# Performance work log

Measured on AMD Instinct MI355X. Metric: run time of the kernel, lower is better.

The kernel has to match this reference:

```python
import jax, jax.numpy as jnp
import numpy as np

N_NODES = 100000
N_EDGES = 3200000
D_IN, D_HID, N_CLASSES = 128, 16, 10


def gcn_conv(x, src, dst, W, b, num_nodes):
    # PyG GCNConv: h = W x; add self-loops; symmetric deg^-1/2 normalization; scatter-sum; + bias
    h = x @ W                                        # [N, d_out]
    loops = jnp.arange(num_nodes, dtype=src.dtype)
    s = jnp.concatenate([src, loops])                # [E+N]
    d = jnp.concatenate([dst, loops])                # [E+N]
    deg = jax.ops.segment_sum(jnp.ones_like(d, dtype=h.dtype), d, num_segments=num_nodes)
    dinv = jax.lax.rsqrt(jnp.maximum(deg, 1.0))      # self-loops guarantee deg >= 1
    norm = dinv[s] * dinv[d]                         # [E+N]
    msg = h[s] * norm[:, None]                       # gather + scale
    out = jax.ops.segment_sum(msg, d, num_segments=num_nodes)
    return out + b


def setup_inputs() -> dict:
    key = jax.random.key(0)
    k1, k2, k3, k4, k5, k6 = jax.random.split(key, 6)
    x = jax.random.normal(k1, (N_NODES, D_IN), dtype=jnp.float32)
    edge_index = jax.random.randint(k2, (2, N_EDGES), 0, N_NODES, dtype=jnp.int32)
    W1 = jax.random.normal(k3, (D_IN, D_HID), dtype=jnp.float32) / np.sqrt(D_IN)
    b1 = jnp.zeros((D_HID,), dtype=jnp.float32)
    W2 = jax.random.normal(k4, (D_HID, N_CLASSES), dtype=jnp.float32) / np.sqrt(D_HID)
    b2 = jnp.zeros((N_CLASSES,), dtype=jnp.float32)
    return {"x": x, "edge_index": edge_index, "W1": W1, "b1": b1, "W2": W2, "b2": b2}


def reference(x, edge_index, W1, b1, W2, b2):
    num_nodes = x.shape[0]
    src, dst = edge_index[0], edge_index[1]
    h = jax.nn.relu(gcn_conv(x, src, dst, W1, b1, num_nodes))
    # dropout is identity in eval mode
    h = gcn_conv(h, src, dst, W2, b2, num_nodes)
    return jax.nn.log_softmax(h, axis=1)
```

## Files before the change

kernel.cpp:

```cpp
#include <hip/hip_runtime.h>
#include <hip/hip_fp16.h>
#include <math.h>

#define NNODES 100000
#define BSH 7
#define NBUCK 782
#define CAP 5120
#define EPB 8192
#define PBT 512
#define EPT 16

typedef __attribute__((ext_vector_type(8))) _Float16 f16x8;
typedef __attribute__((ext_vector_type(2))) __fp16 fp16x2;
typedef __attribute__((ext_vector_type(4))) float f32x4;

__device__ inline __half2 shfl_xor_h2(__half2 v, int m) {
    union { __half2 h; int i; } u;
    u.h = v;
    u.i = __shfl_xor(u.i, m);
    return u.h;
}

__global__ void k_zero(int* __restrict__ p, int n) {
    int t = threadIdx.x;
    if (t < n) p[t] = 0;
}

__global__ __launch_bounds__(512) void k_part(const int* __restrict__ src, const int* __restrict__ dst,
                                              int* __restrict__ bcur, unsigned int* __restrict__ part,
                                              int E) {
    __shared__ int h[NBUCK];
    __shared__ int gb[NBUCK];
    int t = threadIdx.x;
    for (int i = t; i < NBUCK; i += PBT) h[i] = 0;
    __syncthreads();
    int base = blockIdx.x * EPB;
    int n = min(EPB, E - base);
    const int2* src2 = (const int2*)(src + base);
    const int2* dst2 = (const int2*)(dst + base);
    unsigned ev[EPT];
    int bv[EPT];
#pragma unroll
    for (int p = 0; p < EPT / 2; ++p) {
        int i2 = t + p * PBT;
        if (2 * i2 < n) {
            int2 s2 = src2[i2];
            int2 d2 = dst2[i2];
            bv[2 * p]     = d2.x >> BSH;
            ev[2 * p]     = (unsigned)s2.x | ((unsigned)(d2.x & 127) << 17);
            bv[2 * p + 1] = d2.y >> BSH;
            ev[2 * p + 1] = (unsigned)s2.y | ((unsigned)(d2.y & 127) << 17);
            atomicAdd(&h[bv[2 * p]], 1);
            atomicAdd(&h[bv[2 * p + 1]], 1);
        } else {
            bv[2 * p] = -1;
            bv[2 * p + 1] = -1;
        }
    }
    __syncthreads();
    for (int bq = t; bq < NBUCK; bq += PBT) {
        int c = h[bq];
        if (c) gb[bq] = atomicAdd(&bcur[bq], c);
        h[bq] = 0;
    }
    __syncthreads();
#pragma unroll
    for (int p = 0; p < EPT; ++p) {
        if (bv[p] >= 0) {
            int pos = atomicAdd(&h[bv[p]], 1);
            int g = gb[bv[p]] + pos;
            if (g < CAP) part[(size_t)bv[p] * CAP + g] = ev[p];
        }
    }
}

__global__ __launch_bounds__(256) void k_build(unsigned int* __restrict__ part,
                                               const int* __restrict__ bcur,
                                               int* __restrict__ cnt, int* __restrict__ off,
                                               float* __restrict__ dinv,
                                               const float* __restrict__ x, const float* __restrict__ W1,
                                               __half* __restrict__ h1s, int n_nodes) {
    __shared__ int lcnt[128], lscan[128], lcur[128];
    __shared__ float sdinv[128];
    __shared__ _Float16 sWT[16 * 136];
    __shared__ unsigned int lraw[CAP];
    int t = threadIdx.x;
    int b = blockIdx.x;
    int ec = min(bcur[b], CAP);
    size_t base = (size_t)b * CAP;
    if (t < 128) lcnt[t] = 0;
    for (int i = t; i < 2048; i += 256) {
        int k = i >> 4, j = i & 15;
        sWT[j * 136 + k] = (_Float16)W1[i];
    }
    __syncthreads();
    for (int i = t; i < ec; i += 256) {
        unsigned v = part[base + i];
        lraw[i] = v;
        atomicAdd(&lcnt[v >> 17], 1);
    }
    __syncthreads();
    if (t < 128) lscan[t] = lcnt[t];
    __syncthreads();
    for (int d = 1; d < 128; d <<= 1) {
        int v = (t >= d && t < 128) ? lscan[t - d] : 0;
        __syncthreads();
        if (t < 128) lscan[t] += v;
        __syncthreads();
    }
    if (t < 128) {
        int ex = lscan[t] - lcnt[t];
        lcur[t] = ex;
        int node = (b << BSH) + t;
        float dv = rsqrtf((float)(lcnt[t] + 1));
        sdinv[t] = dv;
        if (node < NNODES) {
            off[node] = (int)base + ex;
            cnt[node] = lcnt[t];
            dinv[node] = dv;
        }
    }
    __syncthreads();
    for (int i = t; i < ec; i += 256) {
        unsigned v = lraw[i];
        int p = atomicAdd(&lcur[v >> 17], 1);
        part[base + p] = v & 0x1FFFFu;
    }
    int w = t >> 6, lane = t & 63;
    int row = lane & 15, kg = lane >> 4;
#pragma unroll
    for (int it = 0; it < 2; ++it) {
        int node0 = (b << BSH) + it * 64 + w * 16;
        if (node0 < n_nodes) {
            int n = node0 + row;
            const float* xp = x + (size_t)min(n, n_nodes - 1) * 128 + kg * 8;
            const _Float16* wp = &sWT[row * 136 + kg * 8];
            f32x4 acc = {0.f, 0.f, 0.f, 0.f};
#pragma unroll
            for (int s = 0; s < 4; ++s) {
                float4 xa = *(const float4*)(xp + s * 32);
                float4 xb = *(const float4*)(xp + s * 32 + 4);
                union { f16x8 v8; fp16x2 v2[4]; } A;
                A.v2[0] = __builtin_amdgcn_cvt_pkrtz(xa.x, xa.y);
                A.v2[1] = __builtin_amdgcn_cvt_pkrtz(xa.z, xa.w);
                A.v2[2] = __builtin_amdgcn_cvt_pkrtz(xb.x, xb.y);
                A.v2[3] = __builtin_amdgcn_cvt_pkrtz(xb.z, xb.w);
                f16x8 B = *(const f16x8*)(wp + s * 32);
                acc = __builtin_amdgcn_mfma_f32_16x16x32_f16(A.v8, B, acc, 0, 0, 0);
            }
#pragma unroll
            for (int i = 0; i < 4; ++i) {
                int r = kg * 4 + i;
                int nn = node0 + r;
                if (nn < n_nodes) {
                    float dn = sdinv[it * 64 + w * 16 + r];
                    h1s[(size_t)nn * 16 + row] = __float2half(acc[i] * dn);
                }
            }
        }
    }
}

__global__ __launch_bounds__(256) void k_agg1(const __half* __restrict__ h1s, const unsigned int* __restrict__ col,
                                              const int* __restrict__ off, const int* __restrict__ cnt,
                                              const float* __restrict__ dinv, const float* __restrict__ b1,
                                              const float* __restrict__ W2, __half* __restrict__ h3s,
                                              int n_nodes) {
    __shared__ float sW2[16 * 17];
    __shared__ float sB[16];
    int t = threadIdx.x;
    {
        int k = t >> 4, jj = t & 15;
        sW2[k * 17 + jj] = (jj < 10) ? W2[k * 10 + jj] : 0.f;
    }
    if (t < 16) sB[t] = b1[t];
    __syncthreads();
    int wid = (blockIdx.x * 256 + t) >> 3;
    if (wid >= n_nodes) return;
    int lane = t & 63;
    int fg = lane & 1, sl = (lane >> 1) & 3;
    int deg = cnt[wid], o = off[wid];
    __half2 a0 = __floats2half2_rn(0.f, 0.f), a1 = a0, a2 = a0, a3 = a0;
    int e = sl;
    int s_cur = (e < deg) ? (int)col[o + e] : 0;
    while (e < deg) {
        int en = e + 4;
        int s_nxt = (en < deg) ? (int)col[o + en] : 0;
        uint4 u = *(const uint4*)(h1s + (size_t)s_cur * 16 + fg * 8);
        a0 = __hadd2(a0, *(__half2*)&u.x);
        a1 = __hadd2(a1, *(__half2*)&u.y);
        a2 = __hadd2(a2, *(__half2*)&u.z);
        a3 = __hadd2(a3, *(__half2*)&u.w);
        s_cur = s_nxt;
        e = en;
    }
#pragma unroll
    for (int m = 2; m <= 4; m <<= 1) {
        a0 = __hadd2(a0, shfl_xor_h2(a0, m));
        a1 = __hadd2(a1, shfl_xor_h2(a1, m));
        a2 = __hadd2(a2, shfl_xor_h2(a2, m));
        a3 = __hadd2(a3, shfl_xor_h2(a3, m));
    }
    {
        uint4 u = *(const uint4*)(h1s + (size_t)wid * 16 + fg * 8);
        a0 = __hadd2(a0, *(__half2*)&u.x);
        a1 = __hadd2(a1, *(__half2*)&u.y);
        a2 = __hadd2(a2, *(__half2*)&u.z);
        a3 = __hadd2(a3, *(__half2*)&u.w);
    }
    float2 f01 = __half22float2(a0), f23 = __half22float2(a1);
    float2 f45 = __half22float2(a2), f67 = __half22float2(a3);
    float f[8] = {f01.x, f01.y, f23.x, f23.y, f45.x, f45.y, f67.x, f67.y};
    float dn = dinv[wid];
    int k0 = fg * 8;
    float hv[8];
#pragma unroll
    for (int i = 0; i < 8; ++i) hv[i] = fmaxf(fmaf(dn, f[i], sB[k0 + i]), 0.f);
    float p[4];
#pragma unroll
    for (int c = 0; c < 4; ++c) {
        float acc = 0.f;
#pragma unroll
        for (int i = 0; i < 8; ++i) acc = fmaf(hv[i], sW2[(k0 + i) * 17 + sl * 4 + c], acc);
        acc += __shfl_xor(acc, 1);
        p[c] = acc * dn;
    }
    if (fg == 0) {
        __half2 w0 = __floats2half2_rn(p[0], p[1]);
        __half2 w1 = __floats2half2_rn(p[2], p[3]);
        union { __half2 h[2]; uint2 u; } pk;
        pk.h[0] = w0; pk.h[1] = w1;
        *(uint2*)(h3s + (size_t)wid * 16 + sl * 4) = pk.u;
    }
}

__global__ __launch_bounds__(256) void k_agg2(const __half* __restrict__ h3s, const unsigned int* __restrict__ col,
                                              const int* __restrict__ off, const int* __restrict__ cnt,
                                              const float* __restrict__ dinv, const float* __restrict__ b2,
                                              float* __restrict__ out, int n_nodes) {
    int t = threadIdx.x;
    int wid = (blockIdx.x * 256 + t) >> 3;
    if (wid >= n_nodes) return;
    int lane = t & 63;
    int fg = lane & 1, sl = (lane >> 1) & 3;
    int deg = cnt[wid], o = off[wid];
    __half2 a0 = __floats2half2_rn(0.f, 0.f), a1 = a0, a2 = a0, a3 = a0;
    int e = sl;
    int s_cur = (e < deg) ? (int)col[o + e] : 0;
    while (e < deg) {
        int en = e + 4;
        int s_nxt = (en < deg) ? (int)col[o + en] : 0;
        uint4 u = *(const uint4*)(h3s + (size_t)s_cur * 16 + fg * 8);
        a0 = __hadd2(a0, *(__half2*)&u.x);
        a1 = __hadd2(a1, *(__half2*)&u.y);
        a2 = __hadd2(a2, *(__half2*)&u.z);
        a3 = __hadd2(a3, *(__half2*)&u.w);
        s_cur = s_nxt;
        e = en;
    }
#pragma unroll
    for (int m = 2; m <= 4; m <<= 1) {
        a0 = __hadd2(a0, shfl_xor_h2(a0, m));
        a1 = __hadd2(a1, shfl_xor_h2(a1, m));
        a2 = __hadd2(a2, shfl_xor_h2(a2, m));
        a3 = __hadd2(a3, shfl_xor_h2(a3, m));
    }
    {
        uint4 u = *(const uint4*)(h3s + (size_t)wid * 16 + fg * 8);
        a0 = __hadd2(a0, *(__half2*)&u.x);
        a1 = __hadd2(a1, *(__half2*)&u.y);
        a2 = __hadd2(a2, *(__half2*)&u.z);
        a3 = __hadd2(a3, *(__half2*)&u.w);
    }
    float2 f01 = __half22float2(a0), f23 = __half22float2(a1);
    float2 f45 = __half22float2(a2), f67 = __half22float2(a3);
    float f[8] = {f01.x, f01.y, f23.x, f23.y, f45.x, f45.y, f67.x, f67.y};
    float dn = dinv[wid];
    float v[8];
    float mx = -1e30f;
#pragma unroll
    for (int i = 0; i < 8; ++i) {
        int idx = fg * 8 + i;
        if (idx < 10) {
            v[i] = fmaf(dn, f[i], b2[idx]);
            mx = fmaxf(mx, v[i]);
        } else v[i] = 0.f;
    }
    mx = fmaxf(mx, __shfl_xor(mx, 1));
    float se = 0.f;
#pragma unroll
    for (int i = 0; i < 8; ++i) {
        int idx = fg * 8 + i;
        if (idx < 10) se += __expf(v[i] - mx);
    }
    se += __shfl_xor(se, 1);
    float lse = mx + __logf(se);
    if (sl == 0) {
#pragma unroll
        for (int i = 0; i < 8; ++i) {
            int idx = fg * 8 + i;
            if (idx < 10) out[(size_t)wid * 10 + idx] = v[i] - lse;
        }
    }
}


extern "C" void kernel_launch(void* const* d_in, const int* in_sizes, int n_in,
                              void* d_out, int out_size, void* d_ws, size_t ws_size,
                              hipStream_t stream) {
    const float* x  = (const float*)d_in[0];
    const int*   ei = (const int*)d_in[1];
    const float* W1 = (const float*)d_in[2];
    const float* b1 = (const float*)d_in[3];
    const float* W2 = (const float*)d_in[4];
    const float* b2 = (const float*)d_in[5];
    float* out = (float*)d_out;

    const int N = in_sizes[0] / 128;
    const int E = in_sizes[1] / 2;
    const int* src = ei;
    const int* dst = ei + E;

    char* ws = (char*)d_ws;
    size_t o = 0;
    auto alloc = [&](size_t bytes) {
        size_t p = o;
        o = (o + bytes + 255) & ~(size_t)255;
        return p;
    };
    int*    bcur = (int*)(ws + alloc(1024 * 4));
    int*    cnt  = (int*)(ws + alloc((size_t)N * 4));
    int*    off  = (int*)(ws + alloc((size_t)N * 4));
    float*  dinv = (float*)(ws + alloc((size_t)N * 4));
    unsigned int* part = (unsigned int*)(ws + alloc((size_t)NBUCK * CAP * 4));
    __half* h1s  = (__half*)(ws + alloc((size_t)N * 16 * 2));
    __half* h3s  = (__half*)(ws + alloc((size_t)N * 16 * 2));

    k_zero<<<1, 1024, 0, stream>>>(bcur, 1024);

    int gp = (E + EPB - 1) / EPB;
    k_part<<<gp, PBT, 0, stream>>>(src, dst, bcur, part, E);
    k_build<<<NBUCK, 256, 0, stream>>>(part, bcur, cnt, off, dinv, x, W1, h1s, N);

    int ga = (N * 8 + 255) / 256;
    k_agg1<<<ga, 256, 0, stream>>>(h1s, part, off, cnt, dinv, b1, W2, h3s, N);
    k_agg2<<<ga, 256, 0, stream>>>(h3s, part, off, cnt, dinv, b2, out, N);
}
```

Baseline: 117.7 us.

## Prefetch x rows early, split LDS histogram, use wave-shuffle scan in k_build

The x feature loads for the fused GEMM now start at kernel entry and sit in 64 registers, so their latency overlaps the bucket counting and scatter phases. The LDS histogram counters are split by thread parity to reduce atomic contention, with a second cursor set for the scatter. The block-wide Hillis-Steele scan, which needed many __syncthreads, is replaced by a wave-level __shfl_up scan plus a cross-wave fixup. The cost is much higher register pressure in k_build, which may lower occupancy.

```diff
diff --git a/kernel.cpp b/kernel.cpp
--- a/kernel.cpp
+++ b/kernel.cpp
@@ -80,7 +80,9 @@
                                                float* __restrict__ dinv,
                                                const float* __restrict__ x, const float* __restrict__ W1,
                                                __half* __restrict__ h1s, int n_nodes) {
-    __shared__ int lcnt[128], lscan[128], lcur[128];
+    __shared__ int lcnt[256];
+    __shared__ int lsc[128];
+    __shared__ int lcur[256];
     __shared__ float sdinv[128];
     __shared__ _Float16 sWT[16 * 136];
     __shared__ unsigned int lraw[CAP];
@@ -88,58 +90,80 @@
     int b = blockIdx.x;
     int ec = min(bcur[b], CAP);
     size_t base = (size_t)b * CAP;
-    if (t < 128) lcnt[t] = 0;
+    int w = t >> 6, lane = t & 63;
+    int row = lane & 15, kg = lane >> 4;
+
+    float4 xv[16];
+    {
+        int n0 = (b << BSH) + w * 16 + row;
+        int n1 = n0 + 64;
+        const float* xp0 = x + (size_t)min(n0, n_nodes - 1) * 128 + kg * 8;
+        const float* xp1 = x + (size_t)min(n1, n_nodes - 1) * 128 + kg * 8;
+#pragma unroll
+        for (int s = 0; s < 4; ++s) {
+            xv[s * 2 + 0] = *(const float4*)(xp0 + s * 32);
+            xv[s * 2 + 1] = *(const float4*)(xp0 + s * 32 + 4);
+            xv[8 + s * 2 + 0] = *(const float4*)(xp1 + s * 32);
+            xv[8 + s * 2 + 1] = *(const float4*)(xp1 + s * 32 + 4);
+        }
+    }
+    lcnt[t] = 0;
     for (int i = t; i < 2048; i += 256) {
         int k = i >> 4, j = i & 15;
         sWT[j * 136 + k] = (_Float16)W1[i];
     }
     __syncthreads();
+    int par = (t & 1) << 7;
     for (int i = t; i < ec; i += 256) {
         unsigned v = part[base + i];
         lraw[i] = v;
-        atomicAdd(&lcnt[v >> 17], 1);
-    }
-    __syncthreads();
-    if (t < 128) lscan[t] = lcnt[t];
-    __syncthreads();
-    for (int d = 1; d < 128; d <<= 1) {
-        int v = (t >= d && t < 128) ? lscan[t - d] : 0;
-        __syncthreads();
-        if (t < 128) lscan[t] += v;
-        __syncthreads();
-    }
+        atomicAdd(&lcnt[par + (v >> 17)], 1);
+    }
+    __syncthreads();
     if (t < 128) {
-        int ex = lscan[t] - lcnt[t];
+        int ce = lcnt[t], co = lcnt[128 + t];
+        int c = ce + co;
+        int val = c;
+#pragma unroll
+        for (int d = 1; d < 64; d <<= 1) {
+            int u = __shfl_up(val, d);
+            if (lane >= d) val += u;
+        }
+        lsc[t] = val;
+    }
+    __syncthreads();
+    if (t < 128) {
+        int ce = lcnt[t];
+        int c = ce + lcnt[128 + t];
+        int incl = lsc[t] + ((t >= 64) ? lsc[63] : 0);
+        int ex = incl - c;
         lcur[t] = ex;
+        lcur[128 + t] = ex + ce;
         int node = (b << BSH) + t;
-        float dv = rsqrtf((float)(lcnt[t] + 1));
+        float dv = rsqrtf((float)(c + 1));
         sdinv[t] = dv;
         if (node < NNODES) {
             off[node] = (int)base + ex;
-            cnt[node] = lcnt[t];
+            cnt[node] = c;
             dinv[node] = dv;
         }
     }
     __syncthreads();
     for (int i = t; i < ec; i += 256) {
         unsigned v = lraw[i];
-        int p = atomicAdd(&lcur[v >> 17], 1);
+        int p = atomicAdd(&lcur[par + (v >> 17)], 1);
         part[base + p] = v & 0x1FFFFu;
     }
-    int w = t >> 6, lane = t & 63;
-    int row = lane & 15, kg = lane >> 4;
 #pragma unroll
     for (int it = 0; it < 2; ++it) {
         int node0 = (b << BSH) + it * 64 + w * 16;
         if (node0 < n_nodes) {
-            int n = node0 + row;
-            const float* xp = x + (size_t)min(n, n_nodes - 1) * 128 + kg * 8;
             const _Float16* wp = &sWT[row * 136 + kg * 8];
             f32x4 acc = {0.f, 0.f, 0.f, 0.f};
 #pragma unroll
             for (int s = 0; s < 4; ++s) {
-                float4 xa = *(const float4*)(xp + s * 32);
-                float4 xb = *(const float4*)(xp + s * 32 + 4);
+                float4 xa = xv[it * 8 + s * 2];
+                float4 xb = xv[it * 8 + s * 2 + 1];
                 union { f16x8 v8; fp16x2 v2[4]; } A;
                 A.v2[0] = __builtin_amdgcn_cvt_pkrtz(xa.x, xa.y);
                 A.v2[1] = __builtin_amdgcn_cvt_pkrtz(xa.z, xa.w);
```

After: 119.1 us. No clear change (+1.2%).

## Split CSR build into two half-bucket blocks writing to separate column array

Applied to the files above, without the earlier changes.

k_build now launches two blocks per bucket, each handling 64 of the 128 destination nodes. Each block scans the whole bucket window but counts and scatters only its own half, writing into a new col array instead of rewriting part in place. The per-block prefix scan moves from a shared-memory loop with barriers to a wavefront shuffle scan, and the large lraw shared staging buffer is removed. This doubles parallelism and cuts shared memory per block, at the cost of each block reading its bucket twice from global memory and a per-half capacity limit (HCAP) that silently drops edges when one half exceeds 2560.

```diff
diff --git a/kernel.cpp b/kernel.cpp
--- a/kernel.cpp
+++ b/kernel.cpp
@@ -6,6 +6,7 @@
 #define BSH 7
 #define NBUCK 782
 #define CAP 5120
+#define HCAP 2560
 #define EPB 8192
 #define PBT 512
 #define EPT 16
@@ -74,88 +75,89 @@
     }
 }
 
-__global__ __launch_bounds__(256) void k_build(unsigned int* __restrict__ part,
+__global__ __launch_bounds__(256) void k_build(const unsigned int* __restrict__ part,
                                                const int* __restrict__ bcur,
                                                int* __restrict__ cnt, int* __restrict__ off,
-                                               float* __restrict__ dinv,
+                                               float* __restrict__ dinv, unsigned int* __restrict__ col,
                                                const float* __restrict__ x, const float* __restrict__ W1,
                                                __half* __restrict__ h1s, int n_nodes) {
-    __shared__ int lcnt[128], lscan[128], lcur[128];
-    __shared__ float sdinv[128];
+    __shared__ int lcnt[64], lcur[64];
+    __shared__ float sdinv[64];
     __shared__ _Float16 sWT[16 * 136];
-    __shared__ unsigned int lraw[CAP];
-    int t = threadIdx.x;
-    int b = blockIdx.x;
+    int t = threadIdx.x;
+    int b = blockIdx.x >> 1, half = blockIdx.x & 1;
     int ec = min(bcur[b], CAP);
-    size_t base = (size_t)b * CAP;
-    if (t < 128) lcnt[t] = 0;
+    const unsigned int* window = part + (size_t)b * CAP;
+    int gbase = b * CAP + half * HCAP;
+
+    if (t < 64) lcnt[t] = 0;
     for (int i = t; i < 2048; i += 256) {
         int k = i >> 4, j = i & 15;
         sWT[j * 136 + k] = (_Float16)W1[i];
     }
     __syncthreads();
     for (int i = t; i < ec; i += 256) {
-        unsigned v = part[base + i];
-        lraw[i] = v;
-        atomicAdd(&lcnt[v >> 17], 1);
-    }
-    __syncthreads();
-    if (t < 128) lscan[t] = lcnt[t];
-    __syncthreads();
-    for (int d = 1; d < 128; d <<= 1) {
-        int v = (t >= d && t < 128) ? lscan[t - d] : 0;
-        __syncthreads();
-        if (t < 128) lscan[t] += v;
-        __syncthreads();
-    }
-    if (t < 128) {
-        int ex = lscan[t] - lcnt[t];
+        unsigned v = window[i];
+        int dl = (int)(v >> 17);
+        if ((dl >> 6) == half) atomicAdd(&lcnt[dl & 63], 1);
+    }
+    __syncthreads();
+    if (t < 64) {
+        int c = lcnt[t];
+        int val = c;
+#pragma unroll
+        for (int d = 1; d < 64; d <<= 1) {
+            int u = __shfl_up(val, d);
+            if (t >= d) val += u;
+        }
+        int ex = val - c;
         lcur[t] = ex;
-        int node = (b << BSH) + t;
-        float dv = rsqrtf((float)(lcnt[t] + 1));
+        int node = (b << BSH) + half * 64 + t;
+        float dv = rsqrtf((float)(c + 1));
         sdinv[t] = dv;
         if (node < NNODES) {
-            off[node] = (int)base + ex;
-            cnt[node] = lcnt[t];
+            off[node] = gbase + ex;
+            cnt[node] = c;
             dinv[node] = dv;
         }
     }
     __syncthreads();
+    unsigned int* colw = col + gbase;
     for (int i = t; i < ec; i += 256) {
-        unsigned v = lraw[i];
-        int p = atomicAdd(&lcur[v >> 17], 1);
-        part[base + p] = v & 0x1FFFFu;
+        unsigned v = window[i];
+        int dl = (int)(v >> 17);
+        if ((dl >> 6) == half) {
+            int p = atomicAdd(&lcur[dl & 63], 1);
+            if (p < HCAP) colw[p] = v & 0x1FFFFu;
+        }
     }
     int w = t >> 6, lane = t & 63;
     int row = lane & 15, kg = lane >> 4;
-#pragma unroll
-    for (int it = 0; it < 2; ++it) {
-        int node0 = (b << BSH) + it * 64 + w * 16;
-        if (node0 < n_nodes) {
-            int n = node0 + row;
-            const float* xp = x + (size_t)min(n, n_nodes - 1) * 128 + kg * 8;
-            const _Float16* wp = &sWT[row * 136 + kg * 8];
-            f32x4 acc = {0.f, 0.f, 0.f, 0.f};
-#pragma unroll
-            for (int s = 0; s < 4; ++s) {
-                float4 xa = *(const float4*)(xp + s * 32);
-                float4 xb = *(const float4*)(xp + s * 32 + 4);
-                union { f16x8 v8; fp16x2 v2[4]; } A;
-                A.v2[0] = __builtin_amdgcn_cvt_pkrtz(xa.x, xa.y);
-                A.v2[1] = __builtin_amdgcn_cvt_pkrtz(xa.z, xa.w);
-                A.v2[2] = __builtin_amdgcn_cvt_pkrtz(xb.x, xb.y);
-                A.v2[3] = __builtin_amdgcn_cvt_pkrtz(xb.z, xb.w);
-                f16x8 B = *(const f16x8*)(wp + s * 32);
-                acc = __builtin_amdgcn_mfma_f32_16x16x32_f16(A.v8, B, acc, 0, 0, 0);
-            }
-#pragma unroll
-            for (int i = 0; i < 4; ++i) {
-                int r = kg * 4 + i;
-                int nn = node0 + r;
-                if (nn < n_nodes) {
-                    float dn = sdinv[it * 64 + w * 16 + r];
-                    h1s[(size_t)nn * 16 + row] = __float2half(acc[i] * dn);
-                }
+    int node0 = (b << BSH) + half * 64 + w * 16;
+    if (node0 < n_nodes) {
+        int n = node0 + row;
+        const float* xp = x + (size_t)min(n, n_nodes - 1) * 128 + kg * 8;
+        const _Float16* wp = &sWT[row * 136 + kg * 8];
+        f32x4 acc = {0.f, 0.f, 0.f, 0.f};
+#pragma unroll
+        for (int s = 0; s < 4; ++s) {
+            float4 xa = *(const float4*)(xp + s * 32);
+            float4 xb = *(const float4*)(xp + s * 32 + 4);
+            union { f16x8 v8; fp16x2 v2[4]; } A;
+            A.v2[0] = __builtin_amdgcn_cvt_pkrtz(xa.x, xa.y);
+            A.v2[1] = __builtin_amdgcn_cvt_pkrtz(xa.z, xa.w);
+            A.v2[2] = __builtin_amdgcn_cvt_pkrtz(xb.x, xb.y);
+            A.v2[3] = __builtin_amdgcn_cvt_pkrtz(xb.z, xb.w);
+            f16x8 B = *(const f16x8*)(wp + s * 32);
+            acc = __builtin_amdgcn_mfma_f32_16x16x32_f16(A.v8, B, acc, 0, 0, 0);
+        }
+#pragma unroll
+        for (int i = 0; i < 4; ++i) {
+            int r = kg * 4 + i;
+            int nn = node0 + r;
+            if (nn < n_nodes) {
+                float dn = sdinv[half * 0 + w * 16 + r];
+                h1s[(size_t)nn * 16 + row] = __float2half(acc[i] * dn);
             }
         }
     }
@@ -333,6 +335,7 @@
     int*    off  = (int*)(ws + alloc((size_t)N * 4));
     float*  dinv = (float*)(ws + alloc((size_t)N * 4));
     unsigned int* part = (unsigned int*)(ws + alloc((size_t)NBUCK * CAP * 4));
+    unsigned int* col  = (unsigned int*)(ws + alloc((size_t)NBUCK * CAP * 4));
     __half* h1s  = (__half*)(ws + alloc((size_t)N * 16 * 2));
     __half* h3s  = (__half*)(ws + alloc((size_t)N * 16 * 2));
 
@@ -340,9 +343,9 @@
 
     int gp = (E + EPB - 1) / EPB;
     k_part<<<gp, PBT, 0, stream>>>(src, dst, bcur, part, E);
-    k_build<<<NBUCK, 256, 0, stream>>>(part, bcur, cnt, off, dinv, x, W1, h1s, N);
+    k_build<<<NBUCK * 2, 256, 0, stream>>>(part, bcur, cnt, off, dinv, col, x, W1, h1s, N);
 
     int ga = (N * 8 + 255) / 256;
-    k_agg1<<<ga, 256, 0, stream>>>(h1s, part, off, cnt, dinv, b1, W2, h3s, N);
-    k_agg2<<<ga, 256, 0, stream>>>(h3s, part, off, cnt, dinv, b2, out, N);
-}
+    k_agg1<<<ga, 256, 0, stream>>>(h1s, col, off, cnt, dinv, b1, W2, h3s, N);
+    k_agg2<<<ga, 256, 0, stream>>>(h3s, col, off, cnt, dinv, b2, out, N);
+}
```

After: 123.4 us. +4.8%, slower.

## Move X·W1 GEMM into partition kernel blocks and apply dinv scaling in build

Applied to the files above, without the earlier changes.

Adds extra blocks to the edge-partition kernel that compute the unscaled x@W1 projection with MFMA, so the dense GEMM runs alongside the partitioning work rather than after it inside k_build. k_build then only rescales the stored fp16 rows in place by dinv. The aim is to overlap the memory-bound x read with the atomic-heavy partition phase and shorten k_build. In exchange, h1 is written and read once more, and an extra fp16 rounding is applied before scaling.

```diff
diff --git a/kernel.cpp b/kernel.cpp
--- a/kernel.cpp
+++ b/kernel.cpp
@@ -9,6 +9,7 @@
 #define EPB 8192
 #define PBT 512
 #define EPT 16
+#define GP 391
 
 typedef __attribute__((ext_vector_type(8))) _Float16 f16x8;
 typedef __attribute__((ext_vector_type(2))) __fp16 fp16x2;
@@ -26,50 +27,87 @@
     if (t < n) p[t] = 0;
 }
 
-__global__ __launch_bounds__(512) void k_part(const int* __restrict__ src, const int* __restrict__ dst,
-                                              int* __restrict__ bcur, unsigned int* __restrict__ part,
-                                              int E) {
-    __shared__ int h[NBUCK];
-    __shared__ int gb[NBUCK];
-    int t = threadIdx.x;
-    for (int i = t; i < NBUCK; i += PBT) h[i] = 0;
-    __syncthreads();
-    int base = blockIdx.x * EPB;
-    int n = min(EPB, E - base);
-    const int2* src2 = (const int2*)(src + base);
-    const int2* dst2 = (const int2*)(dst + base);
-    unsigned ev[EPT];
-    int bv[EPT];
-#pragma unroll
-    for (int p = 0; p < EPT / 2; ++p) {
-        int i2 = t + p * PBT;
-        if (2 * i2 < n) {
-            int2 s2 = src2[i2];
-            int2 d2 = dst2[i2];
-            bv[2 * p]     = d2.x >> BSH;
-            ev[2 * p]     = (unsigned)s2.x | ((unsigned)(d2.x & 127) << 17);
-            bv[2 * p + 1] = d2.y >> BSH;
-            ev[2 * p + 1] = (unsigned)s2.y | ((unsigned)(d2.y & 127) << 17);
-            atomicAdd(&h[bv[2 * p]], 1);
-            atomicAdd(&h[bv[2 * p + 1]], 1);
-        } else {
-            bv[2 * p] = -1;
-            bv[2 * p + 1] = -1;
-        }
-    }
-    __syncthreads();
-    for (int bq = t; bq < NBUCK; bq += PBT) {
-        int c = h[bq];
-        if (c) gb[bq] = atomicAdd(&bcur[bq], c);
-        h[bq] = 0;
-    }
-    __syncthreads();
-#pragma unroll
-    for (int p = 0; p < EPT; ++p) {
-        if (bv[p] >= 0) {
-            int pos = atomicAdd(&h[bv[p]], 1);
-            int g = gb[bv[p]] + pos;
-            if (g < CAP) part[(size_t)bv[p] * CAP + g] = ev[p];
+__global__ __launch_bounds__(512) void k_pg(const int* __restrict__ src, const int* __restrict__ dst,
+                                            int* __restrict__ bcur, unsigned int* __restrict__ part,
+                                            const float* __restrict__ x, const float* __restrict__ W1,
+                                            __half* __restrict__ h1, int E, int n_nodes) {
+    __shared__ __align__(16) int smem[2 * NBUCK];
+    int t = threadIdx.x;
+    if (blockIdx.x < GP) {
+        int* h = smem;
+        int* gbv = smem + NBUCK;
+        for (int i = t; i < NBUCK; i += PBT) h[i] = 0;
+        __syncthreads();
+        int base = blockIdx.x * EPB;
+        int n = min(EPB, E - base);
+        const int2* src2 = (const int2*)(src + base);
+        const int2* dst2 = (const int2*)(dst + base);
+        unsigned ev[EPT];
+        int bv[EPT];
+#pragma unroll
+        for (int p = 0; p < EPT / 2; ++p) {
+            int i2 = t + p * PBT;
+            if (2 * i2 < n) {
+                int2 s2 = src2[i2];
+                int2 d2 = dst2[i2];
+                bv[2 * p]     = d2.x >> BSH;
+                ev[2 * p]     = (unsigned)s2.x | ((unsigned)(d2.x & 127) << 17);
+                bv[2 * p + 1] = d2.y >> BSH;
+                ev[2 * p + 1] = (unsigned)s2.y | ((unsigned)(d2.y & 127) << 17);
+                atomicAdd(&h[bv[2 * p]], 1);
+                atomicAdd(&h[bv[2 * p + 1]], 1);
+            } else {
+                bv[2 * p] = -1;
+                bv[2 * p + 1] = -1;
+            }
+        }
+        __syncthreads();
+        for (int bq = t; bq < NBUCK; bq += PBT) {
+            int c = h[bq];
+            if (c) gbv[bq] = atomicAdd(&bcur[bq], c);
+            h[bq] = 0;
+        }
+        __syncthreads();
+#pragma unroll
+        for (int p = 0; p < EPT; ++p) {
+            if (bv[p] >= 0) {
+                int pos = atomicAdd(&h[bv[p]], 1);
+                int g = gbv[bv[p]] + pos;
+                if (g < CAP) part[(size_t)bv[p] * CAP + g] = ev[p];
+            }
+        }
+    } else {
+        _Float16* sWT = (_Float16*)smem;
+        for (int i = t; i < 2048; i += 512) {
+            int k = i >> 4, j = i & 15;
+            sWT[j * 136 + k] = (_Float16)W1[i];
+        }
+        __syncthreads();
+        int w = t >> 6, lane = t & 63;
+        int row = lane & 15, kg = lane >> 4;
+        int node0 = (blockIdx.x - GP) * 128 + w * 16;
+        if (node0 >= n_nodes) return;
+        int n = node0 + row;
+        const float* xp = x + (size_t)min(n, n_nodes - 1) * 128 + kg * 8;
+        const _Float16* wp = &sWT[row * 136 + kg * 8];
+        f32x4 acc = {0.f, 0.f, 0.f, 0.f};
+#pragma unroll
+        for (int s = 0; s < 4; ++s) {
+            float4 xa = *(const float4*)(xp + s * 32);
+            float4 xb = *(const float4*)(xp + s * 32 + 4);
+            union { f16x8 v8; fp16x2 v2[4]; } A;
+            A.v2[0] = __builtin_amdgcn_cvt_pkrtz(xa.x, xa.y);
+            A.v2[1] = __builtin_amdgcn_cvt_pkrtz(xa.z, xa.w);
+            A.v2[2] = __builtin_amdgcn_cvt_pkrtz(xb.x, xb.y);
+            A.v2[3] = __builtin_amdgcn_cvt_pkrtz(xb.z, xb.w);
+            f16x8 B = *(const f16x8*)(wp + s * 32);
+            acc = __builtin_amdgcn_mfma_f32_16x16x32_f16(A.v8, B, acc, 0, 0, 0);
+        }
+#pragma unroll
+        for (int i = 0; i < 4; ++i) {
+            int r = kg * 4 + i;
+            int nn = node0 + r;
+            if (nn < n_nodes) h1[(size_t)nn * 16 + row] = __float2half(acc[i]);
         }
     }
 }
@@ -77,22 +115,16 @@
 __global__ __launch_bounds__(256) void k_build(unsigned int* __restrict__ part,
                                                const int* __restrict__ bcur,
                                                int* __restrict__ cnt, int* __restrict__ off,
-                                               float* __restrict__ dinv,
-                                               const float* __restrict__ x, const float* __restrict__ W1,
-                                               __half* __restrict__ h1s, int n_nodes) {
+                                               float* __restrict__ dinv, __half* __restrict__ h1,
+                                               int n_nodes) {
     __shared__ int lcnt[128], lscan[128], lcur[128];
     __shared__ float sdinv[128];
-    __shared__ _Float16 sWT[16 * 136];
     __shared__ unsigned int lraw[CAP];
     int t = threadIdx.x;
     int b = blockIdx.x;
     int ec = min(bcur[b], CAP);
     size_t base = (size_t)b * CAP;
     if (t < 128) lcnt[t] = 0;
-    for (int i = t; i < 2048; i += 256) {
-        int k = i >> 4, j = i & 15;
-        sWT[j * 136 + k] = (_Float16)W1[i];
-    }
     __syncthreads();
     for (int i = t; i < ec; i += 256) {
         unsigned v = part[base + i];
@@ -126,37 +158,21 @@
         int p = atomicAdd(&lcur[v >> 17], 1);
         part[base + p] = v & 0x1FFFFu;
     }
-    int w = t >> 6, lane = t & 63;
-    int row = lane & 15, kg = lane >> 4;
-#pragma unroll
-    for (int it = 0; it < 2; ++it) {
-        int node0 = (b << BSH) + it * 64 + w * 16;
-        if (node0 < n_nodes) {
-            int n = node0 + row;
-            const float* xp = x + (size_t)min(n, n_nodes - 1) * 128 + kg * 8;
-            const _Float16* wp = &sWT[row * 136 + kg * 8];
-            f32x4 acc = {0.f, 0.f, 0.f, 0.f};
-#pragma unroll
-            for (int s = 0; s < 4; ++s) {
-                float4 xa = *(const float4*)(xp + s * 32);
-                float4 xb = *(const float4*)(xp + s * 32 + 4);
-                union { f16x8 v8; fp16x2 v2[4]; } A;
-                A.v2[0] = __builtin_amdgcn_cvt_pkrtz(xa.x, xa.y);
-                A.v2[1] = __builtin_amdgcn_cvt_pkrtz(xa.z, xa.w);
-                A.v2[2] = __builtin_amdgcn_cvt_pkrtz(xb.x, xb.y);
-                A.v2[3] = __builtin_amdgcn_cvt_pkrtz(xb.z, xb.w);
-                f16x8 B = *(const f16x8*)(wp + s * 32);
-                acc = __builtin_amdgcn_mfma_f32_16x16x32_f16(A.v8, B, acc, 0, 0, 0);
+    {
+        int nd = t >> 1, qq = t & 1;
+        int node = (b << BSH) + nd;
+        if (node < n_nodes) {
+            float dn = sdinv[nd];
+            uint4* p4 = (uint4*)(h1 + (size_t)node * 16 + qq * 8);
+            uint4 v = *p4;
+            union { __half2 hh[4]; uint4 u; } U;
+            U.u = v;
+#pragma unroll
+            for (int q = 0; q < 4; ++q) {
+                float2 f = __half22float2(U.hh[q]);
+                U.hh[q] = __floats2half2_rn(f.x * dn, f.y * dn);
             }
-#pragma unroll
-            for (int i = 0; i < 4; ++i) {
-                int r = kg * 4 + i;
-                int nn = node0 + r;
-                if (nn < n_nodes) {
-                    float dn = sdinv[it * 64 + w * 16 + r];
-                    h1s[(size_t)nn * 16 + row] = __float2half(acc[i] * dn);
-                }
-            }
+            *p4 = U.u;
         }
     }
 }
@@ -338,9 +354,9 @@
 
     k_zero<<<1, 1024, 0, stream>>>(bcur, 1024);
 
-    int gp = (E + EPB - 1) / EPB;
-    k_part<<<gp, PBT, 0, stream>>>(src, dst, bcur, part, E);
-    k_build<<<NBUCK, 256, 0, stream>>>(part, bcur, cnt, off, dinv, x, W1, h1s, N);
+    int gg = (N + 127) / 128;
+    k_pg<<<GP + gg, PBT, 0, stream>>>(src, dst, bcur, part, x, W1, h1s, E, N);
+    k_build<<<NBUCK, 256, 0, stream>>>(part, bcur, cnt, off, dinv, h1s, N);
 
     int ga = (N * 8 + 255) / 256;
     k_agg1<<<ga, 256, 0, stream>>>(h1s, part, off, cnt, dinv, b1, W2, h3s, N);
```

Result: no change. 118.9 us (+1.0%).
